# Performance work log

Hardware: AMD Instinct MI355X
Metric: run time of the kernel (lower is better)

Reference implementation:

```python
import jax, jax.numpy as jnp
import numpy as np
import math

D_MODEL = 1024
N_HEADS = 16
Q_PROJ = D_MODEL // 4
KV_PROJ = D_MODEL // 4
DH = D_MODEL // N_HEADS
LN_EPS = 1e-5


def _layernorm(x, gamma, beta):
    mu = jnp.mean(x, axis=-1, keepdims=True)
    var = jnp.mean(jnp.square(x - mu), axis=-1, keepdims=True)
    return (x - mu) * jax.lax.rsqrt(var + LN_EPS) * gamma + beta


def setup_inputs() -> dict:
    key = jax.random.key(0)
    ks = jax.random.split(key, 7)
    B, S = 2, 2048
    x = jax.random.normal(ks[0], (B, S, D_MODEL), dtype=jnp.float32)
    W_dq = 0.01 * jax.random.normal(ks[1], (D_MODEL, Q_PROJ), dtype=jnp.float32)
    W_uq = 0.01 * jax.random.normal(ks[2], (Q_PROJ, D_MODEL), dtype=jnp.float32)
    W_dkv = 0.01 * jax.random.normal(ks[3], (D_MODEL, KV_PROJ), dtype=jnp.float32)
    W_ukv = 0.01 * jax.random.normal(ks[4], (KV_PROJ, 2 * D_MODEL), dtype=jnp.float32)
    W_o = 0.01 * jax.random.normal(ks[5], (D_MODEL, D_MODEL), dtype=jnp.float32)
    return {
        "x": x,
        "W_dq": W_dq, "W_uq": W_uq,
        "q_ln_g": jnp.ones((Q_PROJ,), jnp.float32), "q_ln_b": jnp.zeros((Q_PROJ,), jnp.float32),
        "W_dkv": W_dkv, "W_ukv": W_ukv,
        "kv_ln_g": jnp.ones((KV_PROJ,), jnp.float32), "kv_ln_b": jnp.zeros((KV_PROJ,), jnp.float32),
        "W_o": W_o,
    }


def reference(x, W_dq, W_uq, q_ln_g, q_ln_b, W_dkv, W_ukv, kv_ln_g, kv_ln_b, W_o):
    B, S, D = x.shape
    # low-rank Q path
    cq = _layernorm(x @ W_dq, q_ln_g, q_ln_b)          # [B,S,q_proj]
    Q = cq @ W_uq                                       # [B,S,D]
    # low-rank KV path
    ckv = _layernorm(x @ W_dkv, kv_ln_g, kv_ln_b)       # [B,S,kv_proj]
    KV = ckv @ W_ukv                                    # [B,S,2D]
    K, V = KV[..., :D], KV[..., D:]
    q = Q.reshape(B, S, N_HEADS, DH)
    k = K.reshape(B, S, N_HEADS, DH)
    v = V.reshape(B, S, N_HEADS, DH)
    scores = jnp.einsum("bqhd,bkhd->bhqk", q, k) / math.sqrt(float(DH))
    # faithful to original: multiply by tril mask, then set exact zeros to -inf
    mask = jnp.tril(jnp.ones((S, S), dtype=scores.dtype))
    scores = scores * mask
    scores = jnp.where(scores == 0, -jnp.inf, scores)
    attn = jax.nn.softmax(scores, axis=-1)
    out = jnp.einsum("bhqk,bkhd->bqhd", attn, v).reshape(B, S, D)
    return out @ W_o.T
```

## Files before the change

### kernel.cpp

```cpp
#include <hip/hip_runtime.h>

typedef __bf16 bf16;
typedef __bf16 bf16x4 __attribute__((ext_vector_type(4)));
typedef __bf16 bf16x8 __attribute__((ext_vector_type(8)));
typedef float f32x4 __attribute__((ext_vector_type(4)));

#define D_MODEL 1024
#define PROJ    256
#define SEQ     2048
#define BATCH   2
#define TOK     4096
#define NH      16
#define DH      64
#define NEG_BIG (-1e30f)
#define QSCALE  0.18033688011112042f

#if __has_builtin(__builtin_amdgcn_exp2f)
#define EXP2(x) __builtin_amdgcn_exp2f(x)
#else
#define EXP2(x) exp2f(x)
#endif

typedef __attribute__((address_space(3))) unsigned int  lds_u32;
typedef __attribute__((address_space(1))) unsigned int  glb_u32;

__device__ __forceinline__ void gl2lds16(const void* gsrc, void* ldst) {
    __builtin_amdgcn_global_load_lds((const glb_u32*)gsrc, (lds_u32*)ldst, 16, 0, 0);
}

#define VM_WAIT(N) asm volatile("s_waitcnt vmcnt(" #N ")" ::: "memory")
#define LGKM0      asm volatile("s_waitcnt lgkmcnt(0)" ::: "memory")
#define SCHEDB()   __builtin_amdgcn_sched_barrier(0)
#define SBAR()     __builtin_amdgcn_s_barrier()

template <int CTRL>
__device__ __forceinline__ float dppmov(float x) {
    int i = __builtin_bit_cast(int, x);
    i = __builtin_amdgcn_update_dpp(i, i, CTRL, 0xf, 0xf, false);
    return __builtin_bit_cast(float, i);
}
__device__ __forceinline__ float rowsum16(float v) {
    v += dppmov<0xB1>(v);
    v += dppmov<0x4E>(v);
    v += dppmov<0x141>(v);
    v += dppmov<0x140>(v);
    return v;
}

__global__ __launch_bounds__(256) void prep_kernel(
    const float* __restrict__ W_o, const float* __restrict__ x,
    const float* __restrict__ W_dq, const float* __restrict__ W_dkv,
    const float* __restrict__ W_uq, const float* __restrict__ W_ukv,
    bf16* __restrict__ Wo16, bf16* __restrict__ x16,
    bf16* __restrict__ Wt_dq, bf16* __restrict__ Wt_dkv,
    bf16* __restrict__ Wt_uq, bf16* __restrict__ Wt_ukv) {
    if (blockIdx.x < 320) {
        __shared__ float tile[64][65];
        int t = blockIdx.x;
        const float* src; bf16* dst; int R, C;
        if (t < 64)       { src = W_dq;  dst = Wt_dq;  R = 1024; C = 256; }
        else if (t < 128) { src = W_dkv; dst = Wt_dkv; R = 1024; C = 256;  t -= 64; }
        else if (t < 192) { src = W_uq;  dst = Wt_uq;  R = 256;  C = 1024; t -= 128; }
        else              { src = W_ukv; dst = Wt_ukv; R = 256;  C = 2048; t -= 192; }
        const int tilesC = C >> 6;
        const int r0 = (t / tilesC) << 6;
        const int c0 = (t % tilesC) << 6;
        const int tr = threadIdx.x >> 6;
        const int tc = threadIdx.x & 63;
#pragma unroll
        for (int i = 0; i < 16; ++i)
            tile[tr * 16 + i][tc] = src[(size_t)(r0 + tr * 16 + i) * C + c0 + tc];
        __syncthreads();
#pragma unroll
        for (int i = 0; i < 16; ++i)
            dst[(size_t)(c0 + tr * 16 + i) * R + r0 + tc] =
                (bf16)tile[tc][tr * 16 + i];
    } else {
        const int NW = 262144;
        const int NX = 1048576;
        for (int i = (blockIdx.x - 320) * 256 + threadIdx.x; i < NW + NX;
             i += 1024 * 256) {
            if (i < NW) {
                float4 v = ((const float4*)W_o)[i];
                bf16x4 p;
                p[0] = (bf16)v.x; p[1] = (bf16)v.y;
                p[2] = (bf16)v.z; p[3] = (bf16)v.w;
                ((bf16x4*)Wo16)[i] = p;
            } else {
                int j = i - NW;
                float4 v = ((const float4*)x)[j];
                bf16x4 p;
                p[0] = (bf16)v.x; p[1] = (bf16)v.y;
                p[2] = (bf16)v.z; p[3] = (bf16)v.w;
                ((bf16x4*)x16)[j] = p;
            }
        }
    }
}

__global__ __launch_bounds__(256) void gemm_ln_kernel(
    const bf16* __restrict__ x16,
    const bf16* __restrict__ Wt_q, const bf16* __restrict__ Wt_kv,
    const float* __restrict__ q_g, const float* __restrict__ q_b,
    const float* __restrict__ kv_g, const float* __restrict__ kv_b,
    bf16* __restrict__ cq, bf16* __restrict__ ckv) {
    __shared__ alignas(16) bf16 xA[2][16 * 32];
    __shared__ alignas(16) bf16 wB[2][256 * 32];
    __shared__ float red1[4][16];
    __shared__ float red2[4][16];

    const int K = 1024;
    const bf16* Wt = blockIdx.y ? Wt_kv : Wt_q;
    const float* gamma = blockIdx.y ? kv_g : q_g;
    const float* beta  = blockIdx.y ? kv_b : q_b;
    bf16* out = blockIdx.y ? ckv : cq;

    const int m0 = blockIdx.x * 16;
    const int wv = threadIdx.x >> 6;
    const int lane = threadIdx.x & 63;
    const int g = lane >> 4;
    const int ln16 = lane & 15;

    const int crow = lane >> 2;
    const int ckc = lane & 3;
    const bf16* gx = x16 + (size_t)(m0 + crow) * K + ckc * 8;
    const bf16* gw = Wt + (size_t)(64 * wv + crow) * K + ckc * 8;

    f32x4 acc[4] = {};
    const int nst = K >> 5;

#pragma unroll
    for (int s = 0; s < 2; ++s) {
        gl2lds16(gx + s * 32, (char*)xA + s * 1024);
#pragma unroll
        for (int i = 0; i < 4; ++i)
            gl2lds16(gw + (size_t)i * 16 * K + s * 32,
                     (char*)wB + s * 16384 + wv * 4096 + i * 1024);
    }
    VM_WAIT(0); SCHEDB(); SBAR();

    for (int s = 0; s < nst; ++s) {
        if (s > 0) {
            if (s + 1 < nst) { VM_WAIT(5); } else { VM_WAIT(0); }
            SCHEDB(); SBAR();
        }
        const bf16* cx = (const bf16*)((const char*)xA + (s & 1) * 1024);
        const bf16* cw = (const bf16*)((const char*)wB + (s & 1) * 16384);
        bf16x8 a = *(const bf16x8*)(cx + ln16 * 32 + g * 8);
        bf16x8 bb[4];
#pragma unroll
        for (int t = 0; t < 4; ++t)
            bb[t] = *(const bf16x8*)(cw + (wv * 64 + 16 * t + ln16) * 32 + g * 8);
        LGKM0; SCHEDB(); SBAR();
        if (s + 2 < nst) {
            const int k2 = (s + 2) * 32;
            gl2lds16(gx + k2, (char*)xA + (s & 1) * 1024);
#pragma unroll
            for (int i = 0; i < 4; ++i)
                gl2lds16(gw + (size_t)i * 16 * K + k2,
                         (char*)wB + (s & 1) * 16384 + wv * 4096 + i * 1024);
        }
        __builtin_amdgcn_s_setprio(1);
#pragma unroll
        for (int t = 0; t < 4; ++t)
            acc[t] = __builtin_amdgcn_mfma_f32_16x16x32_bf16(a, bb[t], acc[t], 0, 0, 0);
        __builtin_amdgcn_s_setprio(0);
    }

    float s1[4], s2[4];
#pragma unroll
    for (int r = 0; r < 4; ++r) {
        float a = 0.f, b = 0.f;
#pragma unroll
        for (int t = 0; t < 4; ++t) { float v = acc[t][r]; a += v; b += v * v; }
        s1[r] = rowsum16(a); s2[r] = rowsum16(b);
    }
    if (ln16 == 0) {
#pragma unroll
        for (int r = 0; r < 4; ++r) {
            red1[wv][g * 4 + r] = s1[r];
            red2[wv][g * 4 + r] = s2[r];
        }
    }
    __syncthreads();
#pragma unroll
    for (int r = 0; r < 4; ++r) {
        int rl = g * 4 + r;
        float t1 = red1[0][rl] + red1[1][rl] + red1[2][rl] + red1[3][rl];
        float t2 = red2[0][rl] + red2[1][rl] + red2[2][rl] + red2[3][rl];
        float mu = t1 * (1.0f / 256.0f);
        float var = t2 * (1.0f / 256.0f) - mu * mu;
        float rs = rsqrtf(var + 1e-5f);
        int row = m0 + rl;
#pragma unroll
        for (int t = 0; t < 4; ++t) {
            int col = wv * 64 + 16 * t + ln16;
            float v = (acc[t][r] - mu) * rs * gamma[col] + beta[col];
            out[(size_t)row * PROJ + col] = (bf16)v;
        }
    }
}

__device__ __forceinline__ void gemm_body128(
    const bf16* __restrict__ A, const bf16* __restrict__ Bt,
    bf16* __restrict__ C, bf16* __restrict__ C2, int K,
    int bx, int by, int mode, bf16* tA, bf16* tB) {
    const int w = threadIdx.x >> 6;
    const int lane = threadIdx.x & 63;
    const int g = lane >> 4;
    const int ln16 = lane & 15;
    const int wr = w >> 1;
    const int wc = w & 1;

    const int m0 = bx * 128;
    const int n0 = by * 128;

    const int crow = lane >> 2;
    const int ckc = lane & 3;
    const bf16* gA0 = A  + (size_t)(m0 + 32 * w + crow) * K + ckc * 8;
    const bf16* gA1 = gA0 + (size_t)16 * K;
    const bf16* gB0 = Bt + (size_t)(n0 + 32 * w + crow) * K + ckc * 8;
    const bf16* gB1 = gB0 + (size_t)16 * K;

    f32x4 acc[4][4] = {};
    const int nst = K >> 5;

#pragma unroll
    for (int s = 0; s < 2; ++s) {
        gl2lds16(gA0 + s * 32, (char*)tA + s * 8192 + w * 2048);
        gl2lds16(gA1 + s * 32, (char*)tA + s * 8192 + w * 2048 + 1024);
        gl2lds16(gB0 + s * 32, (char*)tB + s * 8192 + w * 2048);
        gl2lds16(gB1 + s * 32, (char*)tB + s * 8192 + w * 2048 + 1024);
    }
    VM_WAIT(0); SCHEDB(); SBAR();

    for (int s = 0; s < nst; ++s) {
        if (s > 0) {
            if (s + 1 < nst) { VM_WAIT(4); } else { VM_WAIT(0); }
            SCHEDB(); SBAR();
        }
        const bf16* cA = tA + (s & 1) * 4096;
        const bf16* cB = tB + (s & 1) * 4096;

        bf16x8 af[4], bfr[4];
#pragma unroll
        for (int q = 0; q < 4; ++q)
            af[q] = *(const bf16x8*)(cA + (wr * 64 + q * 16 + ln16) * 32 + g * 8);
#pragma unroll
        for (int t = 0; t < 4; ++t)
            bfr[t] = *(const bf16x8*)(cB + (wc * 64 + t * 16 + ln16) * 32 + g * 8);
        LGKM0; SCHEDB(); SBAR();
        if (s + 2 < nst) {
            const int k2 = (s + 2) * 32;
            gl2lds16(gA0 + k2, (char*)tA + (s & 1) * 8192 + w * 2048);
            gl2lds16(gA1 + k2, (char*)tA + (s & 1) * 8192 + w * 2048 + 1024);
            gl2lds16(gB0 + k2, (char*)tB + (s & 1) * 8192 + w * 2048);
            gl2lds16(gB1 + k2, (char*)tB + (s & 1) * 8192 + w * 2048 + 1024);
        }
        __builtin_amdgcn_s_setprio(1);
#pragma unroll
        for (int q = 0; q < 4; ++q)
#pragma unroll
            for (int t = 0; t < 4; ++t)
                acc[q][t] = __builtin_amdgcn_mfma_f32_16x16x32_bf16(
                    af[q], bfr[t], acc[q][t], 0, 0, 0);
        __builtin_amdgcn_s_setprio(0);
    }

#pragma unroll
    for (int q = 0; q < 4; ++q)
#pragma unroll
        for (int t = 0; t < 4; ++t) {
            const int col = n0 + wc * 64 + t * 16 + ln16;
            const int tok0 = m0 + wr * 64 + q * 16 + g * 4;
            if (mode == 2 && col >= 1024) {
                int cc = col - 1024;
                int h = cc >> 6, d = cc & 63;
                int b = tok0 >> 11, sq = tok0 & 2047;
                bf16x4 pk;
#pragma unroll
                for (int r = 0; r < 4; ++r) pk[r] = (bf16)acc[q][t][r];
                *(bf16x4*)(C2 + ((size_t)((b * 16 + h) * 64 + d) * SEQ + sq)) = pk;
            } else {
#pragma unroll
                for (int r = 0; r < 4; ++r) {
                    int row = tok0 + r;
                    float v = acc[q][t][r];
                    if (mode == 1) v *= QSCALE;
                    int h = col >> 6, d = col & 63;
                    int b = row >> 11, sq = row & 2047;
                    C[((size_t)((b * 16 + h) * 2048 + sq)) * 64 + d] = (bf16)v;
                }
            }
        }
}

__global__ __launch_bounds__(256) void gemm_qkv_kernel(
    const bf16* __restrict__ cq, const bf16* __restrict__ Wt_uq,
    const bf16* __restrict__ ckv, const bf16* __restrict__ Wt_ukv,
    bf16* __restrict__ Qh, bf16* __restrict__ Kh, bf16* __restrict__ Vt) {
    __shared__ alignas(16) bf16 tA[2][128 * 32];
    __shared__ alignas(16) bf16 tB[2][128 * 32];
    const int i = blockIdx.x;
    if (i < 256) {
        gemm_body128(cq, Wt_uq, Qh, nullptr, PROJ,
                     i >> 3, i & 7, 1, &tA[0][0], &tB[0][0]);
    } else {
        const int j = i - 256;
        gemm_body128(ckv, Wt_ukv, Kh, Vt, PROJ,
                     j >> 4, j & 15, 2, &tA[0][0], &tB[0][0]);
    }
}

__device__ __forceinline__ void gemm_body(
    const bf16* __restrict__ A, const bf16* __restrict__ Bt,
    float* __restrict__ C, int N, int K,
    int bx, int by, bf16* tA, bf16* tB) {
    const int w = threadIdx.x >> 6;
    const int lane = threadIdx.x & 63;
    const int g = lane >> 4;
    const int ln16 = lane & 15;
    const int wr = w >> 1;
    const int wc = w & 1;

    const int m0 = bx * 64;
    const int n0 = by * 128;

    const int crow = lane >> 2;
    const int ckc = lane & 3;
    const bf16* gA  = A  + (size_t)(m0 + w * 16 + crow) * K + ckc * 8;
    const bf16* gB0 = Bt + (size_t)(n0 + w * 16 + crow) * K + ckc * 8;
    const bf16* gB1 = Bt + (size_t)(n0 + 64 + w * 16 + crow) * K + ckc * 8;

    f32x4 acc[2][4] = {};
    const int nst = K >> 5;

#pragma unroll
    for (int s = 0; s < 2; ++s) {
        gl2lds16(gA + s * 32, (char*)tA + s * 4096 + w * 1024);
        gl2lds16(gB0 + s * 32, (char*)tB + s * 8192 + w * 1024);
        gl2lds16(gB1 + s * 32, (char*)tB + s * 8192 + 4096 + w * 1024);
    }
    VM_WAIT(0); SCHEDB(); SBAR();

    for (int s = 0; s < nst; ++s) {
        if (s > 0) {
            if (s + 1 < nst) { VM_WAIT(3); } else { VM_WAIT(0); }
            SCHEDB(); SBAR();
        }
        const bf16* cA = tA + (s & 1) * 2048;
        const bf16* cB = tB + (s & 1) * 4096;

        bf16x8 af[2], bfr[4];
#pragma unroll
        for (int q = 0; q < 2; ++q)
            af[q] = *(const bf16x8*)(cA + (wr * 32 + q * 16 + ln16) * 32 + g * 8);
#pragma unroll
        for (int t = 0; t < 4; ++t)
            bfr[t] = *(const bf16x8*)(cB + (wc * 64 + t * 16 + ln16) * 32 + g * 8);
        LGKM0; SCHEDB(); SBAR();
        if (s + 2 < nst) {
            const int k2 = (s + 2) * 32;
            gl2lds16(gA + k2, (char*)tA + (s & 1) * 4096 + w * 1024);
            gl2lds16(gB0 + k2, (char*)tB + (s & 1) * 8192 + w * 1024);
            gl2lds16(gB1 + k2, (char*)tB + (s & 1) * 8192 + 4096 + w * 1024);
        }
        __builtin_amdgcn_s_setprio(1);
#pragma unroll
        for (int q = 0; q < 2; ++q)
#pragma unroll
            for (int t = 0; t < 4; ++t)
                acc[q][t] = __builtin_amdgcn_mfma_f32_16x16x32_bf16(
                    af[q], bfr[t], acc[q][t], 0, 0, 0);
        __builtin_amdgcn_s_setprio(0);
    }

#pragma unroll
    for (int q = 0; q < 2; ++q)
#pragma unroll
        for (int t = 0; t < 4; ++t) {
            const int col = n0 + wc * 64 + t * 16 + ln16;
            const int tok0 = m0 + wr * 32 + q * 16 + g * 4;
#pragma unroll
            for (int r = 0; r < 4; ++r)
                C[(size_t)(tok0 + r) * N + col] = acc[q][t][r];
        }
}

__global__ __launch_bounds__(256) void gemm_o_kernel(
    const bf16* __restrict__ A, const bf16* __restrict__ Bt,
    float* __restrict__ C, int M, int N, int K) {
    __shared__ alignas(16) bf16 tA[2][64 * 32];
    __shared__ alignas(16) bf16 tB[2][128 * 32];
    gemm_body(A, Bt, C, N, K, blockIdx.x, blockIdx.y, &tA[0][0], &tB[0][0]);
}

__device__ __forceinline__ void qk_exp_pack(
    int k0, int q, bool masked, int g, int ln16,
    bf16x8 aq0, bf16x8 aq1, const bf16x8* Kf,
    bf16x8& P1, bf16x8& P2) {
    f32x4 sc[4];
    __builtin_amdgcn_s_setprio(1);
#pragma unroll
    for (int c = 0; c < 4; ++c) {
        f32x4 z = {};
        z = __builtin_amdgcn_mfma_f32_16x16x32_bf16(Kf[2 * c], aq0, z, 0, 0, 0);
        z = __builtin_amdgcn_mfma_f32_16x16x32_bf16(Kf[2 * c + 1], aq1, z, 0, 0, 0);
        sc[c] = z;
    }
    __builtin_amdgcn_s_setprio(0);
    if (masked) {
        const int kb = k0 + 8 * g;
#pragma unroll
        for (int c = 0; c < 4; ++c)
#pragma unroll
            for (int r = 0; r < 4; ++r) {
                int kcol = kb + (c & 1) * 4 + r + ((c >> 1) << 5);
                if (kcol > q) sc[c][r] = NEG_BIG;
            }
    }
#pragma unroll
    for (int c = 0; c < 4; ++c)
#pragma unroll
        for (int r = 0; r < 4; ++r) sc[c][r] = EXP2(sc[c][r]);
#pragma unroll
    for (int r = 0; r < 4; ++r) {
        P1[r] = (bf16)sc[0][r]; P1[4 + r] = (bf16)sc[1][r];
        P2[r] = (bf16)sc[2][r]; P2[4 + r] = (bf16)sc[3][r];
    }
}

__device__ __forceinline__ void pv_accum(
    bf16x8 P1, bf16x8 P2, const bf16x8* Vf, bf16x8 vones,
    f32x4* o, f32x4& oli) {
    __builtin_amdgcn_s_setprio(1);
#pragma unroll
    for (int t = 0; t < 4; ++t) {
        o[t] = __builtin_amdgcn_mfma_f32_16x16x32_bf16(Vf[2 * t], P1, o[t], 0, 0, 0);
        o[t] = __builtin_amdgcn_mfma_f32_16x16x32_bf16(Vf[2 * t + 1], P2, o[t], 0, 0, 0);
    }
    oli = __builtin_amdgcn_mfma_f32_16x16x32_bf16(vones, P1, oli, 0, 0, 0);
    oli = __builtin_amdgcn_mfma_f32_16x16x32_bf16(vones, P2, oli, 0, 0, 0);
    __builtin_amdgcn_s_setprio(0);
}

__global__ __launch_bounds__(128) void attn_kernel(
    const bf16* __restrict__ Qh, const bf16* __restrict__ Kh,
    const bf16* __restrict__ Vt, bf16* __restrict__ AT) {
    __shared__ alignas(128) bf16 kbuf[2][64 * 64];
    __shared__ alignas(128) bf16 vbuf[2][64 * 64];

    const int lane = threadIdx.x & 63;
    const int g = lane >> 4;
    const int ln16 = lane & 15;
    const int wv = threadIdx.x >> 6;

    const int bh = blockIdx.x & 31;
    const int qsuper = 31 - (blockIdx.x >> 5);
    const int nt = qsuper + 1;
    const int qb = qsuper * 64 + wv * 32;

    const bf16* Kbh = Kh + (size_t)bh * SEQ * DH;
    const bf16* Vbh = Vt + (size_t)bh * DH * SEQ;

    const int rho = lane >> 3;
    const int sl  = lane & 7;
    int kofs[4];
    size_t vofs[4];
#pragma unroll
    for (int i = 0; i < 4; ++i) {
        const int row = 32 * wv + 8 * i + rho;
        const int c = sl ^ ((rho & 3) | ((i & 1) << 2));
        kofs[i] = row * 64 + c * 8;
        vofs[i] = (size_t)row * SEQ + c * 8;
    }

    const int row_base = ((ln16 & 12) << 1) + (ln16 & 3);
    int kro[4], vro[4];
#pragma unroll
    for (int c = 0; c < 4; ++c) {
        const int row = row_base + (c & 1) * 4 + ((c >> 1) << 5);
        const int fr = (row & 3) | (((row >> 3) & 1) << 2);
        kro[c] = row * 128 + (g ^ fr) * 16;
    }
#pragma unroll
    for (int t = 0; t < 4; ++t) {
        const int d = 16 * t + ln16;
        const int fd = (d & 3) | (((d >> 3) & 1) << 2);
        vro[t] = d * 128 + (g ^ fd) * 16;
    }

    bf16x8 aq[2][2];
#pragma unroll
    for (int hh = 0; hh < 2; ++hh) {
        const bf16* qp = Qh + ((size_t)bh * SEQ + qb + 16 * hh + ln16) * DH + g * 8;
        aq[hh][0] = *(const bf16x8*)qp;
        aq[hh][1] = *(const bf16x8*)(qp + 32);
    }

    bf16x8 vones;
#pragma unroll
    for (int i = 0; i < 8; ++i) vones[i] = (bf16)1.0f;

    f32x4 o0[4] = {}, o1[4] = {};
    f32x4 oli0 = {}, oli1 = {};

#pragma unroll
    for (int i = 0; i < 4; ++i) {
        gl2lds16(Kbh + kofs[i], (char*)kbuf + wv * 4096 + i * 1024);
        gl2lds16(Vbh + vofs[i], (char*)vbuf + wv * 4096 + i * 1024);
    }
    if (nt > 1) {
#pragma unroll
        for (int i = 0; i < 4; ++i) {
            gl2lds16(Kbh + (size_t)64 * 64 + kofs[i],
                     (char*)kbuf + 8192 + wv * 4096 + i * 1024);
            gl2lds16(Vbh + vofs[i] + 64,
                     (char*)vbuf + 8192 + wv * 4096 + i * 1024);
        }
    }
    VM_WAIT(0); SCHEDB(); SBAR();

    for (int kt = 0; kt < nt; ++kt) {
        if (kt > 0) {
            if (kt + 1 < nt) { VM_WAIT(8); } else { VM_WAIT(0); }
            SCHEDB(); SBAR();
        }
        const char* kb = (const char*)kbuf + (kt & 1) * 8192;
        const char* vb = (const char*)vbuf + (kt & 1) * 8192;
        bf16x8 Kf[8], Vf[8];
#pragma unroll
        for (int c = 0; c < 4; ++c) {
            Kf[2 * c]     = *(const bf16x8*)(kb + kro[c]);
            Kf[2 * c + 1] = *(const bf16x8*)(kb + (kro[c] ^ 64));
        }
#pragma unroll
        for (int t = 0; t < 4; ++t) {
            Vf[2 * t]     = *(const bf16x8*)(vb + vro[t]);
            Vf[2 * t + 1] = *(const bf16x8*)(vb + (vro[t] ^ 64));
        }
        LGKM0; SCHEDB(); SBAR();
        if (kt + 2 < nt) {
            const size_t k0n = (size_t)(kt + 2) * 64;
            char* kd = (char*)kbuf + (kt & 1) * 8192 + wv * 4096;
            char* vd = (char*)vbuf + (kt & 1) * 8192 + wv * 4096;
#pragma unroll
            for (int i = 0; i < 4; ++i) {
                gl2lds16(Kbh + k0n * 64 + kofs[i], kd + i * 1024);
                gl2lds16(Vbh + vofs[i] + k0n, vd + i * 1024);
            }
        }

        const int k0 = kt * 64;
        const bool msk = (kt == qsuper);
        bf16x8 P1a, P2a, P1b, P2b;
        qk_exp_pack(k0, qb + ln16, msk, g, ln16,
                    aq[0][0], aq[0][1], Kf, P1a, P2a);
        qk_exp_pack(k0, qb + 16 + ln16, msk, g, ln16,
                    aq[1][0], aq[1][1], Kf, P1b, P2b);
        pv_accum(P1a, P2a, Vf, vones, o0, oli0);
        pv_accum(P1b, P2b, Vf, vones, o1, oli1);
    }

    const float inv0 = 1.0f / oli0[0];
    const float inv1 = 1.0f / oli1[0];
    const int b = bh >> 4, h = bh & 15;
    const size_t tok0 = (size_t)(b * SEQ + qb + ln16) * D_MODEL + h * DH;
    const size_t tok1 = (size_t)(b * SEQ + qb + 16 + ln16) * D_MODEL + h * DH;
#pragma unroll
    for (int t = 0; t < 4; ++t) {
        bf16x4 pk0, pk1;
#pragma unroll
        for (int r = 0; r < 4; ++r) {
            pk0[r] = (bf16)(o0[t][r] * inv0);
            pk1[r] = (bf16)(o1[t][r] * inv1);
        }
        *(bf16x4*)(AT + tok0 + 16 * t + 4 * g) = pk0;
        *(bf16x4*)(AT + tok1 + 16 * t + 4 * g) = pk1;
    }
}

extern "C" void kernel_launch(void* const* d_in, const int* in_sizes, int n_in,
                              void* d_out, int out_size, void* d_ws, size_t ws_size,
                              hipStream_t stream) {
    const float* x     = (const float*)d_in[0];
    const float* W_dq  = (const float*)d_in[1];
    const float* W_uq  = (const float*)d_in[2];
    const float* q_g   = (const float*)d_in[3];
    const float* q_b   = (const float*)d_in[4];
    const float* W_dkv = (const float*)d_in[5];
    const float* W_ukv = (const float*)d_in[6];
    const float* kv_g  = (const float*)d_in[7];
    const float* kv_b  = (const float*)d_in[8];
    const float* W_o   = (const float*)d_in[9];

    char* ws = (char*)d_ws;
    size_t off = 0;
    bf16* Wo16   = (bf16*)(ws + off); off += (size_t)D_MODEL * D_MODEL * 2;
    bf16* Wt_dq  = (bf16*)(ws + off); off += (size_t)PROJ * D_MODEL * 2;
    bf16* Wt_dkv = (bf16*)(ws + off); off += (size_t)PROJ * D_MODEL * 2;
    bf16* Wt_uq  = (bf16*)(ws + off); off += (size_t)D_MODEL * PROJ * 2;
    bf16* Wt_ukv = (bf16*)(ws + off); off += (size_t)(2 * D_MODEL) * PROJ * 2;
    bf16* x16    = (bf16*)(ws + off); off += (size_t)TOK * D_MODEL * 2;
    bf16* cq     = (bf16*)(ws + off); off += (size_t)TOK * PROJ * 2;
    bf16* ckv    = (bf16*)(ws + off); off += (size_t)TOK * PROJ * 2;
    bf16* Qh     = (bf16*)(ws + off); off += (size_t)TOK * D_MODEL * 2;
    bf16* Kh     = (bf16*)(ws + off); off += (size_t)TOK * D_MODEL * 2;
    bf16* Vt     = (bf16*)(ws + off); off += (size_t)TOK * D_MODEL * 2;
    bf16* AT     = (bf16*)(ws + off); off += (size_t)TOK * D_MODEL * 2;

    prep_kernel<<<1344, 256, 0, stream>>>(
        W_o, x, W_dq, W_dkv, W_uq, W_ukv,
        Wo16, x16, Wt_dq, Wt_dkv, Wt_uq, Wt_ukv);

    gemm_ln_kernel<<<dim3(TOK / 16, 2), 256, 0, stream>>>(
        x16, Wt_dq, Wt_dkv, q_g, q_b, kv_g, kv_b, cq, ckv);

    gemm_qkv_kernel<<<768, 256, 0, stream>>>(cq, Wt_uq, ckv, Wt_ukv, Qh, Kh, Vt);

    attn_kernel<<<1024, 128, 0, stream>>>(Qh, Kh, Vt, AT);

    gemm_o_kernel<<<dim3(TOK / 64, D_MODEL / 128), 256, 0, stream>>>(
        AT, Wo16, (float*)d_out, TOK, D_MODEL, D_MODEL);
}
```

Before: 180.2 us.

## Triple-buffer LDS tiles to drop second barrier; pair causal query blocks in attention

Every GEMM and the attention kernel move from double to triple LDS buffering. The prefetch for step s+2 is now issued before the current tile is read, which removes the extra lgkmcnt wait and barrier per iteration. The attention kernel also gives each block two query superblocks (s and 31-s), so every block does 33 key tiles and causal work is balanced across half as many blocks. The cost is more LDS per block, more live registers for the second Q and accumulator set, and fewer blocks launched for attention.

```diff
diff --git a/kernel.cpp b/kernel.cpp
--- a/kernel.cpp
+++ b/kernel.cpp
@@ -29,7 +29,6 @@
 }
 
 #define VM_WAIT(N) asm volatile("s_waitcnt vmcnt(" #N ")" ::: "memory")
-#define LGKM0      asm volatile("s_waitcnt lgkmcnt(0)" ::: "memory")
 #define SCHEDB()   __builtin_amdgcn_sched_barrier(0)
 #define SBAR()     __builtin_amdgcn_s_barrier()
 
@@ -104,8 +103,8 @@
     const float* __restrict__ q_g, const float* __restrict__ q_b,
     const float* __restrict__ kv_g, const float* __restrict__ kv_b,
     bf16* __restrict__ cq, bf16* __restrict__ ckv) {
-    __shared__ alignas(16) bf16 xA[2][16 * 32];
-    __shared__ alignas(16) bf16 wB[2][256 * 32];
+    __shared__ alignas(16) bf16 xA[3][16 * 32];
+    __shared__ alignas(16) bf16 wB[3][256 * 32];
     __shared__ float red1[4][16];
     __shared__ float red2[4][16];
 
@@ -144,22 +143,22 @@
             if (s + 1 < nst) { VM_WAIT(5); } else { VM_WAIT(0); }
             SCHEDB(); SBAR();
         }
-        const bf16* cx = (const bf16*)((const char*)xA + (s & 1) * 1024);
-        const bf16* cw = (const bf16*)((const char*)wB + (s & 1) * 16384);
+        if (s + 2 < nst) {
+            const int b3 = (s + 2) % 3;
+            const int k2 = (s + 2) * 32;
+            gl2lds16(gx + k2, (char*)xA + b3 * 1024);
+#pragma unroll
+            for (int i = 0; i < 4; ++i)
+                gl2lds16(gw + (size_t)i * 16 * K + k2,
+                         (char*)wB + b3 * 16384 + wv * 4096 + i * 1024);
+        }
+        const bf16* cx = &xA[s % 3][0];
+        const bf16* cw = &wB[s % 3][0];
         bf16x8 a = *(const bf16x8*)(cx + ln16 * 32 + g * 8);
         bf16x8 bb[4];
 #pragma unroll
         for (int t = 0; t < 4; ++t)
             bb[t] = *(const bf16x8*)(cw + (wv * 64 + 16 * t + ln16) * 32 + g * 8);
-        LGKM0; SCHEDB(); SBAR();
-        if (s + 2 < nst) {
-            const int k2 = (s + 2) * 32;
-            gl2lds16(gx + k2, (char*)xA + (s & 1) * 1024);
-#pragma unroll
-            for (int i = 0; i < 4; ++i)
-                gl2lds16(gw + (size_t)i * 16 * K + k2,
-                         (char*)wB + (s & 1) * 16384 + wv * 4096 + i * 1024);
-        }
         __builtin_amdgcn_s_setprio(1);
 #pragma unroll
         for (int t = 0; t < 4; ++t)
@@ -239,8 +238,16 @@
             if (s + 1 < nst) { VM_WAIT(4); } else { VM_WAIT(0); }
             SCHEDB(); SBAR();
         }
-        const bf16* cA = tA + (s & 1) * 4096;
-        const bf16* cB = tB + (s & 1) * 4096;
+        if (s + 2 < nst) {
+            const int b3 = (s + 2) % 3;
+            const int k2 = (s + 2) * 32;
+            gl2lds16(gA0 + k2, (char*)tA + b3 * 8192 + w * 2048);
+            gl2lds16(gA1 + k2, (char*)tA + b3 * 8192 + w * 2048 + 1024);
+            gl2lds16(gB0 + k2, (char*)tB + b3 * 8192 + w * 2048);
+            gl2lds16(gB1 + k2, (char*)tB + b3 * 8192 + w * 2048 + 1024);
+        }
+        const bf16* cA = tA + (s % 3) * 4096;
+        const bf16* cB = tB + (s % 3) * 4096;
 
         bf16x8 af[4], bfr[4];
 #pragma unroll
@@ -249,14 +256,6 @@
 #pragma unroll
         for (int t = 0; t < 4; ++t)
             bfr[t] = *(const bf16x8*)(cB + (wc * 64 + t * 16 + ln16) * 32 + g * 8);
-        LGKM0; SCHEDB(); SBAR();
-        if (s + 2 < nst) {
-            const int k2 = (s + 2) * 32;
-            gl2lds16(gA0 + k2, (char*)tA + (s & 1) * 8192 + w * 2048);
-            gl2lds16(gA1 + k2, (char*)tA + (s & 1) * 8192 + w * 2048 + 1024);
-            gl2lds16(gB0 + k2, (char*)tB + (s & 1) * 8192 + w * 2048);
-            gl2lds16(gB1 + k2, (char*)tB + (s & 1) * 8192 + w * 2048 + 1024);
-        }
         __builtin_amdgcn_s_setprio(1);
 #pragma unroll
         for (int q = 0; q < 4; ++q)
@@ -299,8 +298,8 @@
     const bf16* __restrict__ cq, const bf16* __restrict__ Wt_uq,
     const bf16* __restrict__ ckv, const bf16* __restrict__ Wt_ukv,
     bf16* __restrict__ Qh, bf16* __restrict__ Kh, bf16* __restrict__ Vt) {
-    __shared__ alignas(16) bf16 tA[2][128 * 32];
-    __shared__ alignas(16) bf16 tB[2][128 * 32];
+    __shared__ alignas(16) bf16 tA[3][128 * 32];
+    __shared__ alignas(16) bf16 tB[3][128 * 32];
     const int i = blockIdx.x;
     if (i < 256) {
         gemm_body128(cq, Wt_uq, Qh, nullptr, PROJ,
@@ -348,8 +347,15 @@
             if (s + 1 < nst) { VM_WAIT(3); } else { VM_WAIT(0); }
             SCHEDB(); SBAR();
         }
-        const bf16* cA = tA + (s & 1) * 2048;
-        const bf16* cB = tB + (s & 1) * 4096;
+        if (s + 2 < nst) {
+            const int b3 = (s + 2) % 3;
+            const int k2 = (s + 2) * 32;
+            gl2lds16(gA + k2, (char*)tA + b3 * 4096 + w * 1024);
+            gl2lds16(gB0 + k2, (char*)tB + b3 * 8192 + w * 1024);
+            gl2lds16(gB1 + k2, (char*)tB + b3 * 8192 + 4096 + w * 1024);
+        }
+        const bf16* cA = tA + (s % 3) * 2048;
+        const bf16* cB = tB + (s % 3) * 4096;
 
         bf16x8 af[2], bfr[4];
 #pragma unroll
@@ -358,13 +364,6 @@
 #pragma unroll
         for (int t = 0; t < 4; ++t)
             bfr[t] = *(const bf16x8*)(cB + (wc * 64 + t * 16 + ln16) * 32 + g * 8);
-        LGKM0; SCHEDB(); SBAR();
-        if (s + 2 < nst) {
-            const int k2 = (s + 2) * 32;
-            gl2lds16(gA + k2, (char*)tA + (s & 1) * 4096 + w * 1024);
-            gl2lds16(gB0 + k2, (char*)tB + (s & 1) * 8192 + w * 1024);
-            gl2lds16(gB1 + k2, (char*)tB + (s & 1) * 8192 + 4096 + w * 1024);
-        }
         __builtin_amdgcn_s_setprio(1);
 #pragma unroll
         for (int q = 0; q < 2; ++q)
@@ -390,8 +389,8 @@
 __global__ __launch_bounds__(256) void gemm_o_kernel(
     const bf16* __restrict__ A, const bf16* __restrict__ Bt,
     float* __restrict__ C, int M, int N, int K) {
-    __shared__ alignas(16) bf16 tA[2][64 * 32];
-    __shared__ alignas(16) bf16 tB[2][128 * 32];
+    __shared__ alignas(16) bf16 tA[3][64 * 32];
+    __shared__ alignas(16) bf16 tB[3][128 * 32];
     gemm_body(A, Bt, C, N, K, blockIdx.x, blockIdx.y, &tA[0][0], &tB[0][0]);
 }
 
@@ -444,11 +443,11 @@
     __builtin_amdgcn_s_setprio(0);
 }
 
-__global__ __launch_bounds__(128) void attn_kernel(
+__global__ __launch_bounds__(128, 1) void attn_kernel(
     const bf16* __restrict__ Qh, const bf16* __restrict__ Kh,
     const bf16* __restrict__ Vt, bf16* __restrict__ AT) {
-    __shared__ alignas(128) bf16 kbuf[2][64 * 64];
-    __shared__ alignas(128) bf16 vbuf[2][64 * 64];
+    __shared__ alignas(128) bf16 kbuf[3][64 * 64];
+    __shared__ alignas(128) bf16 vbuf[3][64 * 64];
 
     const int lane = threadIdx.x & 63;
     const int g = lane >> 4;
@@ -456,9 +455,11 @@
     const int wv = threadIdx.x >> 6;
 
     const int bh = blockIdx.x & 31;
-    const int qsuper = 31 - (blockIdx.x >> 5);
-    const int nt = qsuper + 1;
-    const int qb = qsuper * 64 + wv * 32;
+    const int gp = blockIdx.x >> 5;
+    const int sA = 31 - gp;
+    const int sB = gp;
+    const int nA = sA + 1;
+    const int ntot = 33;
 
     const bf16* Kbh = Kh + (size_t)bh * SEQ * DH;
     const bf16* Vbh = Vt + (size_t)bh * DH * SEQ;
@@ -490,60 +491,66 @@
         vro[t] = d * 128 + (g ^ fd) * 16;
     }
 
-    bf16x8 aq[2][2];
+    const int qbA = sA * 64 + wv * 32;
+    const int qbB = sB * 64 + wv * 32;
+    bf16x8 aqA[2][2], aqB[2][2];
 #pragma unroll
     for (int hh = 0; hh < 2; ++hh) {
-        const bf16* qp = Qh + ((size_t)bh * SEQ + qb + 16 * hh + ln16) * DH + g * 8;
-        aq[hh][0] = *(const bf16x8*)qp;
-        aq[hh][1] = *(const bf16x8*)(qp + 32);
-    }
+        const bf16* qpA = Qh + ((size_t)bh * SEQ + qbA + 16 * hh + ln16) * DH + g * 8;
+        const bf16* qpB = Qh + ((size_t)bh * SEQ + qbB + 16 * hh + ln16) * DH + g * 8;
+        aqA[hh][0] = *(const bf16x8*)qpA;
+        aqA[hh][1] = *(const bf16x8*)(qpA + 32);
+        aqB[hh][0] = *(const bf16x8*)qpB;
+        aqB[hh][1] = *(const bf16x8*)(qpB + 32);
+    }
+    bf16x8 ac00 = aqA[0][0], ac01 = aqA[0][1];
+    bf16x8 ac10 = aqA[1][0], ac11 = aqA[1][1];
 
     bf16x8 vones;
 #pragma unroll
     for (int i = 0; i < 8; ++i) vones[i] = (bf16)1.0f;
 
-    f32x4 o0[4] = {}, o1[4] = {};
-    f32x4 oli0 = {}, oli1 = {};
-
-#pragma unroll
-    for (int i = 0; i < 4; ++i) {
-        gl2lds16(Kbh + kofs[i], (char*)kbuf + wv * 4096 + i * 1024);
-        gl2lds16(Vbh + vofs[i], (char*)vbuf + wv * 4096 + i * 1024);
-    }
-    if (nt > 1) {
+    f32x4 oc0[4] = {}, oc1[4] = {};
+    f32x4 os0[4] = {}, os1[4] = {};
+    f32x4 lc0 = {}, lc1 = {}, ls0 = {}, ls1 = {};
+
+    int scur = sA, qbc = qbA;
+
+#pragma unroll
+    for (int s = 0; s < 2; ++s) {
+        char* kd = (char*)kbuf + s * 8192 + wv * 4096;
+        char* vd = (char*)vbuf + s * 8192 + wv * 4096;
 #pragma unroll
         for (int i = 0; i < 4; ++i) {
-            gl2lds16(Kbh + (size_t)64 * 64 + kofs[i],
-                     (char*)kbuf + 8192 + wv * 4096 + i * 1024);
-            gl2lds16(Vbh + vofs[i] + 64,
-                     (char*)vbuf + 8192 + wv * 4096 + i * 1024);
+            gl2lds16(Kbh + (size_t)s * 64 * 64 + kofs[i], kd + i * 1024);
+            gl2lds16(Vbh + vofs[i] + s * 64, vd + i * 1024);
         }
     }
     VM_WAIT(0); SCHEDB(); SBAR();
 
-    for (int kt = 0; kt < nt; ++kt) {
-        if (kt > 0) {
-            if (kt + 1 < nt) { VM_WAIT(8); } else { VM_WAIT(0); }
+    for (int idx = 0; idx < ntot; ++idx) {
+        if (idx > 0) {
+            if (idx + 1 < ntot) { VM_WAIT(8); } else { VM_WAIT(0); }
             SCHEDB(); SBAR();
         }
-        const char* kb = (const char*)kbuf + (kt & 1) * 8192;
-        const char* vb = (const char*)vbuf + (kt & 1) * 8192;
-        bf16x8 Kf[8], Vf[8];
-#pragma unroll
-        for (int c = 0; c < 4; ++c) {
-            Kf[2 * c]     = *(const bf16x8*)(kb + kro[c]);
-            Kf[2 * c + 1] = *(const bf16x8*)(kb + (kro[c] ^ 64));
-        }
-#pragma unroll
-        for (int t = 0; t < 4; ++t) {
-            Vf[2 * t]     = *(const bf16x8*)(vb + vro[t]);
-            Vf[2 * t + 1] = *(const bf16x8*)(vb + (vro[t] ^ 64));
-        }
-        LGKM0; SCHEDB(); SBAR();
-        if (kt + 2 < nt) {
-            const size_t k0n = (size_t)(kt + 2) * 64;
-            char* kd = (char*)kbuf + (kt & 1) * 8192 + wv * 4096;
-            char* vd = (char*)vbuf + (kt & 1) * 8192 + wv * 4096;
+        if (idx == nA) {
+#pragma unroll
+            for (int t = 0; t < 4; ++t) {
+                os0[t] = oc0[t]; os1[t] = oc1[t];
+                oc0[t] = (f32x4){}; oc1[t] = (f32x4){};
+            }
+            ls0 = lc0; ls1 = lc1; lc0 = (f32x4){}; lc1 = (f32x4){};
+            ac00 = aqB[0][0]; ac01 = aqB[0][1];
+            ac10 = aqB[1][0]; ac11 = aqB[1][1];
+            scur = sB; qbc = qbB;
+        }
+        if (idx + 2 < ntot) {
+            const int t2 = idx + 2;
+            const int kt2 = (t2 < nA) ? t2 : t2 - nA;
+            const int b3 = t2 % 3;
+            const size_t k0n = (size_t)kt2 * 64;
+            char* kd = (char*)kbuf + b3 * 8192 + wv * 4096;
+            char* vd = (char*)vbuf + b3 * 8192 + wv * 4096;
 #pragma unroll
             for (int i = 0; i < 4; ++i) {
                 gl2lds16(Kbh + k0n * 64 + kofs[i], kd + i * 1024);
@@ -551,32 +558,64 @@
             }
         }
 
+        const int kt = (idx < nA) ? idx : idx - nA;
+        const char* kb = (const char*)kbuf + (idx % 3) * 8192;
+        const char* vb = (const char*)vbuf + (idx % 3) * 8192;
+        bf16x8 Kf[8], Vf[8];
+#pragma unroll
+        for (int c = 0; c < 4; ++c) {
+            Kf[2 * c]     = *(const bf16x8*)(kb + kro[c]);
+            Kf[2 * c + 1] = *(const bf16x8*)(kb + (kro[c] ^ 64));
+        }
+#pragma unroll
+        for (int t = 0; t < 4; ++t) {
+            Vf[2 * t]     = *(const bf16x8*)(vb + vro[t]);
+            Vf[2 * t + 1] = *(const bf16x8*)(vb + (vro[t] ^ 64));
+        }
+
         const int k0 = kt * 64;
-        const bool msk = (kt == qsuper);
+        const bool msk = (kt == scur);
         bf16x8 P1a, P2a, P1b, P2b;
-        qk_exp_pack(k0, qb + ln16, msk, g, ln16,
-                    aq[0][0], aq[0][1], Kf, P1a, P2a);
-        qk_exp_pack(k0, qb + 16 + ln16, msk, g, ln16,
-                    aq[1][0], aq[1][1], Kf, P1b, P2b);
-        pv_accum(P1a, P2a, Vf, vones, o0, oli0);
-        pv_accum(P1b, P2b, Vf, vones, o1, oli1);
-    }
-
-    const float inv0 = 1.0f / oli0[0];
-    const float inv1 = 1.0f / oli1[0];
+        qk_exp_pack(k0, qbc + ln16, msk, g, ln16, ac00, ac01, Kf, P1a, P2a);
+        qk_exp_pack(k0, qbc + 16 + ln16, msk, g, ln16, ac10, ac11, Kf, P1b, P2b);
+        pv_accum(P1a, P2a, Vf, vones, oc0, lc0);
+        pv_accum(P1b, P2b, Vf, vones, oc1, lc1);
+    }
+
     const int b = bh >> 4, h = bh & 15;
-    const size_t tok0 = (size_t)(b * SEQ + qb + ln16) * D_MODEL + h * DH;
-    const size_t tok1 = (size_t)(b * SEQ + qb + 16 + ln16) * D_MODEL + h * DH;
-#pragma unroll
-    for (int t = 0; t < 4; ++t) {
-        bf16x4 pk0, pk1;
-#pragma unroll
-        for (int r = 0; r < 4; ++r) {
-            pk0[r] = (bf16)(o0[t][r] * inv0);
-            pk1[r] = (bf16)(o1[t][r] * inv1);
-        }
-        *(bf16x4*)(AT + tok0 + 16 * t + 4 * g) = pk0;
-        *(bf16x4*)(AT + tok1 + 16 * t + 4 * g) = pk1;
+    {
+        const float invA0 = 1.0f / ls0[0];
+        const float invA1 = 1.0f / ls1[0];
+        const size_t tokA0 = (size_t)(b * SEQ + qbA + ln16) * D_MODEL + h * DH;
+        const size_t tokA1 = (size_t)(b * SEQ + qbA + 16 + ln16) * D_MODEL + h * DH;
+#pragma unroll
+        for (int t = 0; t < 4; ++t) {
+            bf16x4 p0, p1;
+#pragma unroll
+            for (int r = 0; r < 4; ++r) {
+                p0[r] = (bf16)(os0[t][r] * invA0);
+                p1[r] = (bf16)(os1[t][r] * invA1);
+            }
+            *(bf16x4*)(AT + tokA0 + 16 * t + 4 * g) = p0;
+            *(bf16x4*)(AT + tokA1 + 16 * t + 4 * g) = p1;
+        }
+    }
+    {
+        const float invB0 = 1.0f / lc0[0];
+        const float invB1 = 1.0f / lc1[0];
+        const size_t tokB0 = (size_t)(b * SEQ + qbB + ln16) * D_MODEL + h * DH;
+        const size_t tokB1 = (size_t)(b * SEQ + qbB + 16 + ln16) * D_MODEL + h * DH;
+#pragma unroll
+        for (int t = 0; t < 4; ++t) {
+            bf16x4 p0, p1;
+#pragma unroll
+            for (int r = 0; r < 4; ++r) {
+                p0[r] = (bf16)(oc0[t][r] * invB0);
+                p1[r] = (bf16)(oc1[t][r] * invB1);
+            }
+            *(bf16x4*)(AT + tokB0 + 16 * t + 4 * g) = p0;
+            *(bf16x4*)(AT + tokB1 + 16 * t + 4 * g) = p1;
+        }
     }
 }
 
@@ -618,7 +657,7 @@
 
     gemm_qkv_kernel<<<768, 256, 0, stream>>>(cq, Wt_uq, ckv, Wt_ukv, Qh, Kh, Vt);
 
-    attn_kernel<<<1024, 128, 0, stream>>>(Qh, Kh, Vt, AT);
+    attn_kernel<<<512, 128, 0, stream>>>(Qh, Kh, Vt, AT);
 
     gemm_o_kernel<<<dim3(TOK / 64, D_MODEL / 128), 256, 0, stream>>>(
         AT, Wo16, (float*)d_out, TOK, D_MODEL, D_MODEL);
```

Result: slower. 197.4 us (+9.5%).

## Triple-buffer GEMM LDS stages and load attention V directly from global

Applied to the files above, without the earlier changes.

The GEMM kernels move from double to triple LDS buffering. This lets the prefetch for stage s+2 be issued before the current stage's fragment reads, which removes the second barrier and lgkmcnt wait per K-step. The attention kernel drops the V LDS staging buffer: each lane loads its V fragments straight from global memory into registers, issued before the QK/exp work and waited on just before the PV MFMAs. This cuts LDS traffic and barriers but adds per-lane global latency for V and uses more LDS in the GEMMs, which may lower occupancy.

```diff
diff --git a/kernel.cpp b/kernel.cpp
--- a/kernel.cpp
+++ b/kernel.cpp
@@ -29,7 +29,6 @@
 }
 
 #define VM_WAIT(N) asm volatile("s_waitcnt vmcnt(" #N ")" ::: "memory")
-#define LGKM0      asm volatile("s_waitcnt lgkmcnt(0)" ::: "memory")
 #define SCHEDB()   __builtin_amdgcn_sched_barrier(0)
 #define SBAR()     __builtin_amdgcn_s_barrier()
 
@@ -104,8 +103,8 @@
     const float* __restrict__ q_g, const float* __restrict__ q_b,
     const float* __restrict__ kv_g, const float* __restrict__ kv_b,
     bf16* __restrict__ cq, bf16* __restrict__ ckv) {
-    __shared__ alignas(16) bf16 xA[2][16 * 32];
-    __shared__ alignas(16) bf16 wB[2][256 * 32];
+    __shared__ alignas(16) bf16 xA[3][16 * 32];
+    __shared__ alignas(16) bf16 wB[3][256 * 32];
     __shared__ float red1[4][16];
     __shared__ float red2[4][16];
 
@@ -144,22 +143,22 @@
             if (s + 1 < nst) { VM_WAIT(5); } else { VM_WAIT(0); }
             SCHEDB(); SBAR();
         }
-        const bf16* cx = (const bf16*)((const char*)xA + (s & 1) * 1024);
-        const bf16* cw = (const bf16*)((const char*)wB + (s & 1) * 16384);
+        if (s + 2 < nst) {
+            const int b3 = (s + 2) % 3;
+            const int k2 = (s + 2) * 32;
+            gl2lds16(gx + k2, (char*)xA + b3 * 1024);
+#pragma unroll
+            for (int i = 0; i < 4; ++i)
+                gl2lds16(gw + (size_t)i * 16 * K + k2,
+                         (char*)wB + b3 * 16384 + wv * 4096 + i * 1024);
+        }
+        const bf16* cx = &xA[s % 3][0];
+        const bf16* cw = &wB[s % 3][0];
         bf16x8 a = *(const bf16x8*)(cx + ln16 * 32 + g * 8);
         bf16x8 bb[4];
 #pragma unroll
         for (int t = 0; t < 4; ++t)
             bb[t] = *(const bf16x8*)(cw + (wv * 64 + 16 * t + ln16) * 32 + g * 8);
-        LGKM0; SCHEDB(); SBAR();
-        if (s + 2 < nst) {
-            const int k2 = (s + 2) * 32;
-            gl2lds16(gx + k2, (char*)xA + (s & 1) * 1024);
-#pragma unroll
-            for (int i = 0; i < 4; ++i)
-                gl2lds16(gw + (size_t)i * 16 * K + k2,
-                         (char*)wB + (s & 1) * 16384 + wv * 4096 + i * 1024);
-        }
         __builtin_amdgcn_s_setprio(1);
 #pragma unroll
         for (int t = 0; t < 4; ++t)
@@ -239,8 +238,16 @@
             if (s + 1 < nst) { VM_WAIT(4); } else { VM_WAIT(0); }
             SCHEDB(); SBAR();
         }
-        const bf16* cA = tA + (s & 1) * 4096;
-        const bf16* cB = tB + (s & 1) * 4096;
+        if (s + 2 < nst) {
+            const int b3 = (s + 2) % 3;
+            const int k2 = (s + 2) * 32;
+            gl2lds16(gA0 + k2, (char*)tA + b3 * 8192 + w * 2048);
+            gl2lds16(gA1 + k2, (char*)tA + b3 * 8192 + w * 2048 + 1024);
+            gl2lds16(gB0 + k2, (char*)tB + b3 * 8192 + w * 2048);
+            gl2lds16(gB1 + k2, (char*)tB + b3 * 8192 + w * 2048 + 1024);
+        }
+        const bf16* cA = tA + (s % 3) * 4096;
+        const bf16* cB = tB + (s % 3) * 4096;
 
         bf16x8 af[4], bfr[4];
 #pragma unroll
@@ -249,14 +256,6 @@
 #pragma unroll
         for (int t = 0; t < 4; ++t)
             bfr[t] = *(const bf16x8*)(cB + (wc * 64 + t * 16 + ln16) * 32 + g * 8);
-        LGKM0; SCHEDB(); SBAR();
-        if (s + 2 < nst) {
-            const int k2 = (s + 2) * 32;
-            gl2lds16(gA0 + k2, (char*)tA + (s & 1) * 8192 + w * 2048);
-            gl2lds16(gA1 + k2, (char*)tA + (s & 1) * 8192 + w * 2048 + 1024);
-            gl2lds16(gB0 + k2, (char*)tB + (s & 1) * 8192 + w * 2048);
-            gl2lds16(gB1 + k2, (char*)tB + (s & 1) * 8192 + w * 2048 + 1024);
-        }
         __builtin_amdgcn_s_setprio(1);
 #pragma unroll
         for (int q = 0; q < 4; ++q)
@@ -299,8 +298,8 @@
     const bf16* __restrict__ cq, const bf16* __restrict__ Wt_uq,
     const bf16* __restrict__ ckv, const bf16* __restrict__ Wt_ukv,
     bf16* __restrict__ Qh, bf16* __restrict__ Kh, bf16* __restrict__ Vt) {
-    __shared__ alignas(16) bf16 tA[2][128 * 32];
-    __shared__ alignas(16) bf16 tB[2][128 * 32];
+    __shared__ alignas(16) bf16 tA[3][128 * 32];
+    __shared__ alignas(16) bf16 tB[3][128 * 32];
     const int i = blockIdx.x;
     if (i < 256) {
         gemm_body128(cq, Wt_uq, Qh, nullptr, PROJ,
@@ -348,8 +347,15 @@
             if (s + 1 < nst) { VM_WAIT(3); } else { VM_WAIT(0); }
             SCHEDB(); SBAR();
         }
-        const bf16* cA = tA + (s & 1) * 2048;
-        const bf16* cB = tB + (s & 1) * 4096;
+        if (s + 2 < nst) {
+            const int b3 = (s + 2) % 3;
+            const int k2 = (s + 2) * 32;
+            gl2lds16(gA + k2, (char*)tA + b3 * 4096 + w * 1024);
+            gl2lds16(gB0 + k2, (char*)tB + b3 * 8192 + w * 1024);
+            gl2lds16(gB1 + k2, (char*)tB + b3 * 8192 + 4096 + w * 1024);
+        }
+        const bf16* cA = tA + (s % 3) * 2048;
+        const bf16* cB = tB + (s % 3) * 4096;
 
         bf16x8 af[2], bfr[4];
 #pragma unroll
@@ -358,13 +364,6 @@
 #pragma unroll
         for (int t = 0; t < 4; ++t)
             bfr[t] = *(const bf16x8*)(cB + (wc * 64 + t * 16 + ln16) * 32 + g * 8);
-        LGKM0; SCHEDB(); SBAR();
-        if (s + 2 < nst) {
-            const int k2 = (s + 2) * 32;
-            gl2lds16(gA + k2, (char*)tA + (s & 1) * 4096 + w * 1024);
-            gl2lds16(gB0 + k2, (char*)tB + (s & 1) * 8192 + w * 1024);
-            gl2lds16(gB1 + k2, (char*)tB + (s & 1) * 8192 + 4096 + w * 1024);
-        }
         __builtin_amdgcn_s_setprio(1);
 #pragma unroll
         for (int q = 0; q < 2; ++q)
@@ -390,8 +389,8 @@
 __global__ __launch_bounds__(256) void gemm_o_kernel(
     const bf16* __restrict__ A, const bf16* __restrict__ Bt,
     float* __restrict__ C, int M, int N, int K) {
-    __shared__ alignas(16) bf16 tA[2][64 * 32];
-    __shared__ alignas(16) bf16 tB[2][128 * 32];
+    __shared__ alignas(16) bf16 tA[3][64 * 32];
+    __shared__ alignas(16) bf16 tB[3][128 * 32];
     gemm_body(A, Bt, C, N, K, blockIdx.x, blockIdx.y, &tA[0][0], &tB[0][0]);
 }
 
@@ -448,7 +447,6 @@
     const bf16* __restrict__ Qh, const bf16* __restrict__ Kh,
     const bf16* __restrict__ Vt, bf16* __restrict__ AT) {
     __shared__ alignas(128) bf16 kbuf[2][64 * 64];
-    __shared__ alignas(128) bf16 vbuf[2][64 * 64];
 
     const int lane = threadIdx.x & 63;
     const int g = lane >> 4;
@@ -466,29 +464,26 @@
     const int rho = lane >> 3;
     const int sl  = lane & 7;
     int kofs[4];
-    size_t vofs[4];
 #pragma unroll
     for (int i = 0; i < 4; ++i) {
         const int row = 32 * wv + 8 * i + rho;
         const int c = sl ^ ((rho & 3) | ((i & 1) << 2));
         kofs[i] = row * 64 + c * 8;
-        vofs[i] = (size_t)row * SEQ + c * 8;
     }
 
     const int row_base = ((ln16 & 12) << 1) + (ln16 & 3);
-    int kro[4], vro[4];
+    int kro[4];
 #pragma unroll
     for (int c = 0; c < 4; ++c) {
         const int row = row_base + (c & 1) * 4 + ((c >> 1) << 5);
         const int fr = (row & 3) | (((row >> 3) & 1) << 2);
         kro[c] = row * 128 + (g ^ fr) * 16;
     }
-#pragma unroll
-    for (int t = 0; t < 4; ++t) {
-        const int d = 16 * t + ln16;
-        const int fd = (d & 3) | (((d >> 3) & 1) << 2);
-        vro[t] = d * 128 + (g ^ fd) * 16;
-    }
+
+    const bf16* vp[4];
+#pragma unroll
+    for (int t = 0; t < 4; ++t)
+        vp[t] = Vbh + (size_t)(16 * t + ln16) * SEQ + 8 * g;
 
     bf16x8 aq[2][2];
 #pragma unroll
@@ -505,62 +500,59 @@
     f32x4 o0[4] = {}, o1[4] = {};
     f32x4 oli0 = {}, oli1 = {};
 
-#pragma unroll
-    for (int i = 0; i < 4; ++i) {
-        gl2lds16(Kbh + kofs[i], (char*)kbuf + wv * 4096 + i * 1024);
-        gl2lds16(Vbh + vofs[i], (char*)vbuf + wv * 4096 + i * 1024);
-    }
-    if (nt > 1) {
+    {
+        const int t1 = (nt > 1) ? 1 : 0;
 #pragma unroll
         for (int i = 0; i < 4; ++i) {
-            gl2lds16(Kbh + (size_t)64 * 64 + kofs[i],
+            gl2lds16(Kbh + kofs[i], (char*)kbuf + wv * 4096 + i * 1024);
+            gl2lds16(Kbh + (size_t)t1 * 64 * 64 + kofs[i],
                      (char*)kbuf + 8192 + wv * 4096 + i * 1024);
-            gl2lds16(Vbh + vofs[i] + 64,
-                     (char*)vbuf + 8192 + wv * 4096 + i * 1024);
         }
     }
     VM_WAIT(0); SCHEDB(); SBAR();
 
     for (int kt = 0; kt < nt; ++kt) {
-        if (kt > 0) {
-            if (kt + 1 < nt) { VM_WAIT(8); } else { VM_WAIT(0); }
-            SCHEDB(); SBAR();
-        }
+        if (kt > 0) { SBAR(); }
         const char* kb = (const char*)kbuf + (kt & 1) * 8192;
-        const char* vb = (const char*)vbuf + (kt & 1) * 8192;
-        bf16x8 Kf[8], Vf[8];
+        bf16x8 Kf[8];
 #pragma unroll
         for (int c = 0; c < 4; ++c) {
             Kf[2 * c]     = *(const bf16x8*)(kb + kro[c]);
             Kf[2 * c + 1] = *(const bf16x8*)(kb + (kro[c] ^ 64));
         }
+        asm volatile("s_waitcnt lgkmcnt(0)" ::: "memory");
+        SCHEDB(); SBAR();
+
+        const int k0 = kt * 64;
+        bf16x8 Vf[8];
+        SCHEDB();
 #pragma unroll
         for (int t = 0; t < 4; ++t) {
-            Vf[2 * t]     = *(const bf16x8*)(vb + vro[t]);
-            Vf[2 * t + 1] = *(const bf16x8*)(vb + (vro[t] ^ 64));
-        }
-        LGKM0; SCHEDB(); SBAR();
-        if (kt + 2 < nt) {
-            const size_t k0n = (size_t)(kt + 2) * 64;
+            Vf[2 * t]     = *(const bf16x8*)(vp[t] + k0);
+            Vf[2 * t + 1] = *(const bf16x8*)(vp[t] + k0 + 32);
+        }
+        SCHEDB();
+        {
+            const int kt2 = (kt + 2 < nt) ? kt + 2 : nt - 1;
             char* kd = (char*)kbuf + (kt & 1) * 8192 + wv * 4096;
-            char* vd = (char*)vbuf + (kt & 1) * 8192 + wv * 4096;
-#pragma unroll
-            for (int i = 0; i < 4; ++i) {
-                gl2lds16(Kbh + k0n * 64 + kofs[i], kd + i * 1024);
-                gl2lds16(Vbh + vofs[i] + k0n, vd + i * 1024);
-            }
-        }
-
-        const int k0 = kt * 64;
+#pragma unroll
+            for (int i = 0; i < 4; ++i)
+                gl2lds16(Kbh + (size_t)kt2 * 64 * 64 + kofs[i], kd + i * 1024);
+        }
+        SCHEDB();
+
         const bool msk = (kt == qsuper);
         bf16x8 P1a, P2a, P1b, P2b;
         qk_exp_pack(k0, qb + ln16, msk, g, ln16,
                     aq[0][0], aq[0][1], Kf, P1a, P2a);
         qk_exp_pack(k0, qb + 16 + ln16, msk, g, ln16,
                     aq[1][0], aq[1][1], Kf, P1b, P2b);
+
+        VM_WAIT(4); SCHEDB();
         pv_accum(P1a, P2a, Vf, vones, o0, oli0);
         pv_accum(P1b, P2b, Vf, vones, o1, oli1);
     }
+    VM_WAIT(0);
 
     const float inv0 = 1.0f / oli0[0];
     const float inv1 = 1.0f / oli1[0];
```

Measured after the change: 202.3 us. +12.3%, slower.
